# Kernel optimization log

Measured on AMD Instinct MI355X. Metric: run time of the kernel, lower is better.

The kernel has to match this reference:

```python
import jax, jax.numpy as jnp
import numpy as np

B, D, H, W = 32, 64, 32, 32   # batch, laten_dim, latent spatial dims
K = 2048                      # codebook_size


def setup_inputs() -> dict:
    key = jax.random.key(0)
    k1, k2 = jax.random.split(key)
    laten = jax.random.normal(k1, (B, D, H, W), dtype=jnp.float32)
    codebook = jax.random.normal(k2, (K, D), dtype=jnp.float32)
    return {"laten": laten, "codebook": codebook}


def reference(laten, codebook):
    # Faithful jax translation of VQVAE.quant_laten.
    b, c, h, w = laten.shape
    # (b, c, h, w) -> (b*h*w, c)
    x = jnp.transpose(laten, (0, 2, 3, 1)).reshape(-1, c)  # (N, D)
    # avoids materializing the (N, K, D) broadcast intermediate.
    x_sq = jnp.sum(x * x, axis=-1, keepdims=True)          # (N, 1)
    e_sq = jnp.sum(codebook * codebook, axis=-1)           # (K,)
    l2_distance = (x_sq - 2.0 * (x @ codebook.T) + e_sq) / c  # (N, K)
    closest_idx_2d = jnp.argmin(l2_distance, axis=-1).reshape(b, h, w)
    # gather + permute(0, 3, 1, 2)
    quant_laten = jnp.transpose(codebook[closest_idx_2d], (0, 3, 1, 2))
    return closest_idx_2d, quant_laten
```

## Files before the change

### kernel.cpp

```cpp
#include <hip/hip_runtime.h>

#define N_PIX 32768
#define DIM   64
#define KCODE 2048

typedef __attribute__((ext_vector_type(8))) short bf16x8;
typedef __attribute__((ext_vector_type(4))) float f32x4;

__device__ inline unsigned short f2bf(float v) {
    unsigned int u = __float_as_uint(v);
    return (unsigned short)((u + 0x7FFFu + ((u >> 16) & 1u)) >> 16);
}
__device__ inline float bf2f(unsigned short b) {
    return __uint_as_float(((unsigned int)b) << 16);
}

__global__ __launch_bounds__(256)
void convert_b_kernel(const float* __restrict__ cb, unsigned short* __restrict__ Bg,
                      float* __restrict__ esq) {
    const int t   = blockIdx.x * 256 + threadIdx.x;
    const int n   = t >> 4;
    const int sub = t & 15;
    const int ntile = n >> 4, ni = n & 15;

    const float4 v = *(const float4*)(cb + (size_t)n * DIM + sub * 4);

    unsigned int h01, h23, m01, m23, l01, l23;
    {
        unsigned short h, m, l;
        float r1;
        h = f2bf(v.x); r1 = v.x - bf2f(h); m = f2bf(r1); l = f2bf(r1 - bf2f(m));
        h01 = h;       m01 = m;       l01 = l;
        h = f2bf(v.y); r1 = v.y - bf2f(h); m = f2bf(r1); l = f2bf(r1 - bf2f(m));
        h01 |= (unsigned int)h << 16; m01 |= (unsigned int)m << 16; l01 |= (unsigned int)l << 16;
        h = f2bf(v.z); r1 = v.z - bf2f(h); m = f2bf(r1); l = f2bf(r1 - bf2f(m));
        h23 = h;       m23 = m;       l23 = l;
        h = f2bf(v.w); r1 = v.w - bf2f(h); m = f2bf(r1); l = f2bf(r1 - bf2f(m));
        h23 |= (unsigned int)h << 16; m23 |= (unsigned int)m << 16; l23 |= (unsigned int)l << 16;
    }

    float s = (v.x * v.x + v.y * v.y) + (v.z * v.z + v.w * v.w);
#pragma unroll
    for (int mk = 1; mk < 16; mk <<= 1) s += __shfl_xor(s, mk, 16);
    if (sub == 0) esq[n] = s;

    char* outb = (char*)Bg;
    const size_t u = ((((size_t)ntile) * 8 + (sub >> 1)) << 8) + ni * 16 + (sub & 1) * 8;
    uint2 hw2 = {h01, h23}, mw2 = {m01, m23}, lw2 = {l01, l23};
    *(uint2*)(outb + u)          = hw2;
    *(uint2*)(outb + 262144 + u) = mw2;
    *(uint2*)(outb + 524288 + u) = lw2;
}

#define DO_PASS(APL, BPL)                                                    \
    _Pragma("unroll") for (int ks = 0; ks < 2; ++ks)                         \
    _Pragma("unroll") for (int mt = 0; mt < 2; ++mt)                         \
        acc[mt] = __builtin_amdgcn_mfma_f32_16x16x32_bf16(                   \
            af[APL][mt][ks], bfr[BPL][ks], acc[mt], 0, 0, 0);

#define RELOAD(PL, JN)                                                       \
    if ((JN) < 32) {                                                         \
      const char* gb = bp0 + (size_t)(JN) * 2048 + (size_t)(PL) * 262144;    \
      bfr[PL][0] = *(const bf16x8*)(gb);                                     \
      bfr[PL][1] = *(const bf16x8*)(gb + 1024);                              \
    }

#define ITER(J)                                                              \
  {                                                                          \
    f32x4 acc[2];                                                            \
    acc[0] = f32x4{0.f, 0.f, 0.f, 0.f};                                      \
    acc[1] = f32x4{0.f, 0.f, 0.f, 0.f};                                      \
    __builtin_amdgcn_s_setprio(1);                                           \
    DO_PASS(0, 2)                                                            \
    RELOAD(2, (J) + 1)                                                       \
    DO_PASS(2, 0)                                                            \
    DO_PASS(1, 1)                                                            \
    DO_PASS(0, 1)                                                            \
    RELOAD(1, (J) + 1)                                                       \
    DO_PASS(1, 0)                                                            \
    DO_PASS(0, 0)                                                            \
    RELOAD(0, (J) + 1)                                                       \
    __builtin_amdgcn_s_setprio(0);                                           \
    const int n = wn * 512 + (J) * 16 + col;                                 \
    const float e = esqS[n];                                                 \
    _Pragma("unroll") for (int mt = 0; mt < 2; ++mt)                         \
    _Pragma("unroll") for (int r = 0; r < 4; ++r) {                          \
      float d = fmaf(-2.f, acc[mt][r], e);                                   \
      if (d < best[mt][r]) { best[mt][r] = d; bidx[mt][r] = n; }             \
    }                                                                        \
  }

__global__ __launch_bounds__(512, 4)
void dist_fused_kernel(const float* __restrict__ laten,
                       const unsigned short* __restrict__ Bg,
                       const float* __restrict__ esq,
                       const float* __restrict__ cb,
                       float* __restrict__ out0, float* __restrict__ out1) {
    __shared__ __align__(16) char ring[24576];
    __shared__ float esqS[2048];

    const int tid  = threadIdx.x;
    const int lane = tid & 63;
    const int wave = tid >> 6;
    const int wm   = wave & 1;
    const int wn   = wave >> 1;
    const int quad = lane >> 4, col = lane & 15;
    const int bx = blockIdx.x;
    const int bb = bx >> 4, hw0 = (bx & 15) * 64;

    const char* BgB = (const char*)Bg;
    const char* bp0 = BgB + (size_t)(wn * 32) * 2048 + lane * 16;

    {
        const int p = tid & 63, dg = tid >> 6;
        const float* srcA = laten + (size_t)bb * 65536 + (size_t)dg * 8192 + hw0 + p;
        const int mt = p >> 4, mi = p & 15;
        alignas(16) unsigned short hv[8], mv[8], lv[8];
#pragma unroll
        for (int j = 0; j < 8; ++j) {
            float v = srcA[(size_t)j << 10];
            unsigned short h = f2bf(v);
            float r1 = v - bf2f(h);
            unsigned short m = f2bf(r1);
            unsigned short l = f2bf(r1 - bf2f(m));
            hv[j] = h; mv[j] = m; lv[j] = l;
        }
        int u = ((mt * 8 + dg) << 8) + mi * 16;
        *(uint4*)(ring + u)         = *(uint4*)hv;
        *(uint4*)(ring + 8192 + u)  = *(uint4*)mv;
        *(uint4*)(ring + 16384 + u) = *(uint4*)lv;
    }
    *(float4*)(esqS + tid * 4) = *(const float4*)(esq + tid * 4);
    __syncthreads();

    bf16x8 af[3][2][2];
#pragma unroll
    for (int pl = 0; pl < 3; ++pl)
#pragma unroll
        for (int mt = 0; mt < 2; ++mt)
#pragma unroll
            for (int ks = 0; ks < 2; ++ks)
                af[pl][mt][ks] = *(const bf16x8*)(ring + pl * 8192
                    + (((wm * 2 + mt) * 8 + ks * 4 + quad) << 8) + col * 16);
    __syncthreads();

    bf16x8 bfr[3][2];
    RELOAD(2, 0)
    RELOAD(0, 0)
    RELOAD(1, 0)

    float best[2][4];
    int   bidx[2][4];
#pragma unroll
    for (int mt = 0; mt < 2; ++mt)
#pragma unroll
        for (int r = 0; r < 4; ++r) { best[mt][r] = 3.4e38f; bidx[mt][r] = 0; }

    for (int j = 0; j < 32; ++j) ITER(j)

    float* redD = (float*)ring;
    int*   redI = (int*)(ring + 1024);
    int*   idxF = (int*)(ring + 2048);
#pragma unroll
    for (int mt = 0; mt < 2; ++mt)
#pragma unroll
        for (int r = 0; r < 4; ++r) {
            float d = best[mt][r];
            int   i = bidx[mt][r];
#pragma unroll
            for (int m = 1; m < 16; m <<= 1) {
                float od = __shfl_xor(d, m, 16);
                int   oi = __shfl_xor(i, m, 16);
                if (od < d || (od == d && oi < i)) { d = od; i = oi; }
            }
            if (col == 0) {
                int row = wm * 32 + mt * 16 + quad * 4 + r;
                redD[row * 4 + wn] = d;
                redI[row * 4 + wn] = i;
            }
        }
    __syncthreads();

    if (tid < 64) {
        float bd = redD[tid * 4]; int bi = redI[tid * 4];
#pragma unroll
        for (int w = 1; w < 4; ++w) {
            float d = redD[tid * 4 + w]; int i = redI[tid * 4 + w];
            if (d < bd || (d == bd && i < bi)) { bd = d; bi = i; }
        }
        out0[bx * 64 + tid] = (float)bi;
        idxF[tid] = bi;
    }
    __syncthreads();

    const int p = tid & 63, dg = tid >> 6;
    const int idx = idxF[p];
    const float4* srcr = (const float4*)(cb + ((size_t)idx << 6) + dg * 8);
    float* o = out1 + (size_t)bb * 65536 + (size_t)dg * 8192 + hw0 + p;
    float4 v0 = srcr[0], v1 = srcr[1];
    o[(size_t)0 << 10] = v0.x; o[(size_t)1 << 10] = v0.y;
    o[(size_t)2 << 10] = v0.z; o[(size_t)3 << 10] = v0.w;
    o[(size_t)4 << 10] = v1.x; o[(size_t)5 << 10] = v1.y;
    o[(size_t)6 << 10] = v1.z; o[(size_t)7 << 10] = v1.w;
}

extern "C" void kernel_launch(void* const* d_in, const int* in_sizes, int n_in,
                              void* d_out, int out_size, void* d_ws, size_t ws_size,
                              hipStream_t stream) {
    const float* laten = (const float*)d_in[0];
    const float* cb    = (const float*)d_in[1];

    float* out0 = (float*)d_out;
    float* out1 = (float*)d_out + N_PIX;

    float* esq = (float*)d_ws;
    unsigned short* Bg = (unsigned short*)(esq + 2048);

    convert_b_kernel<<<128, 256, 0, stream>>>(cb, Bg, esq);

    dist_fused_kernel<<<512, 512, 0, stream>>>(laten, Bg, esq, cb, out0, out1);
}
```

Measured before the change: 104.6 us.

## Switch distance GEMM to 32x32x16 MFMA with direct register A-fragment loading

Replaces the 16x16x32 bf16 MFMA tiling with 32x32x16 MFMA, so each wave computes a 32x32 tile per iteration with two split accumulators that are summed before the argmin update. The A operand (split into three bf16 planes) is now built straight into registers from global memory, without staging through a shared-memory ring, which removes one shared-memory round trip and a barrier. Launch bounds occupancy is lowered from 4 to 2 to make room for the larger accumulators and fragments. The argmin reduction is reworked for the 32-lane layout. It trades occupancy and register pressure for fewer MFMA issues and more reuse per instruction.

```diff
diff --git a/kernel.cpp b/kernel.cpp
--- a/kernel.cpp
+++ b/kernel.cpp
@@ -4,8 +4,8 @@
 #define DIM   64
 #define KCODE 2048
 
-typedef __attribute__((ext_vector_type(8))) short bf16x8;
-typedef __attribute__((ext_vector_type(4))) float f32x4;
+typedef __attribute__((ext_vector_type(8)))  short bf16x8;
+typedef __attribute__((ext_vector_type(16))) float f32x16;
 
 __device__ inline unsigned short f2bf(float v) {
     unsigned int u = __float_as_uint(v);
@@ -53,23 +53,21 @@
 }
 
 #define DO_PASS(APL, BPL)                                                    \
-    _Pragma("unroll") for (int ks = 0; ks < 2; ++ks)                         \
-    _Pragma("unroll") for (int mt = 0; mt < 2; ++mt)                         \
-        acc[mt] = __builtin_amdgcn_mfma_f32_16x16x32_bf16(                   \
-            af[APL][mt][ks], bfr[BPL][ks], acc[mt], 0, 0, 0);
+    _Pragma("unroll") for (int ks = 0; ks < 4; ++ks)                         \
+        acc[ks & 1] = __builtin_amdgcn_mfma_f32_32x32x16_bf16(               \
+            af[APL][ks], bfr[BPL][ks], acc[ks & 1], 0, 0, 0);
 
 #define RELOAD(PL, JN)                                                       \
-    if ((JN) < 32) {                                                         \
-      const char* gb = bp0 + (size_t)(JN) * 2048 + (size_t)(PL) * 262144;    \
-      bfr[PL][0] = *(const bf16x8*)(gb);                                     \
-      bfr[PL][1] = *(const bf16x8*)(gb + 1024);                              \
+    if ((JN) < 16) {                                                         \
+      _Pragma("unroll") for (int ks = 0; ks < 4; ++ks)                       \
+        bfr[PL][ks] = *(const bf16x8*)(bp0 + (size_t)(JN) * 4096             \
+                                       + ks * 512 + (size_t)(PL) * 262144);  \
     }
 
 #define ITER(J)                                                              \
   {                                                                          \
-    f32x4 acc[2];                                                            \
-    acc[0] = f32x4{0.f, 0.f, 0.f, 0.f};                                      \
-    acc[1] = f32x4{0.f, 0.f, 0.f, 0.f};                                      \
+    f32x16 acc[2];                                                           \
+    _Pragma("unroll") for (int z = 0; z < 16; ++z) { acc[0][z] = 0.f; acc[1][z] = 0.f; } \
     __builtin_amdgcn_s_setprio(1);                                           \
     DO_PASS(0, 2)                                                            \
     RELOAD(2, (J) + 1)                                                       \
@@ -81,104 +79,94 @@
     DO_PASS(0, 0)                                                            \
     RELOAD(0, (J) + 1)                                                       \
     __builtin_amdgcn_s_setprio(0);                                           \
-    const int n = wn * 512 + (J) * 16 + col;                                 \
-    const float e = esqS[n];                                                 \
-    _Pragma("unroll") for (int mt = 0; mt < 2; ++mt)                         \
-    _Pragma("unroll") for (int r = 0; r < 4; ++r) {                          \
-      float d = fmaf(-2.f, acc[mt][r], e);                                   \
-      if (d < best[mt][r]) { best[mt][r] = d; bidx[mt][r] = n; }             \
+    const int n = wn * 512 + (J) * 32 + (lane & 31);                         \
+    const float e = esqF[n];                                                 \
+    _Pragma("unroll") for (int r = 0; r < 16; ++r) {                         \
+      float s2 = acc[0][r] + acc[1][r];                                      \
+      float d = fmaf(-2.f, s2, e);                                           \
+      if (d < best[r]) { best[r] = d; bidx[r] = n; }                         \
     }                                                                        \
   }
 
-__global__ __launch_bounds__(512, 4)
+__global__ __launch_bounds__(512, 2)
 void dist_fused_kernel(const float* __restrict__ laten,
                        const unsigned short* __restrict__ Bg,
                        const float* __restrict__ esq,
                        const float* __restrict__ cb,
                        float* __restrict__ out0, float* __restrict__ out1) {
-    __shared__ __align__(16) char ring[24576];
-    __shared__ float esqS[2048];
+    __shared__ float esqF[2048];
+    __shared__ float redD[256];
+    __shared__ int   redI[256];
+    __shared__ int   idxF[64];
 
     const int tid  = threadIdx.x;
     const int lane = tid & 63;
     const int wave = tid >> 6;
     const int wm   = wave & 1;
     const int wn   = wave >> 1;
-    const int quad = lane >> 4, col = lane & 15;
+    const int c31  = lane & 31;
+    const int hi   = lane >> 5;
     const int bx = blockIdx.x;
     const int bb = bx >> 4, hw0 = (bx & 15) * 64;
 
     const char* BgB = (const char*)Bg;
-    const char* bp0 = BgB + (size_t)(wn * 32) * 2048 + lane * 16;
-
+    const char* bp0 = BgB + (size_t)wn * 65536 + (size_t)(c31 >> 4) * 2048
+                    + (size_t)hi * 256 + (size_t)(c31 & 15) * 16;
+
+    bf16x8 af[3][4];
     {
-        const int p = tid & 63, dg = tid >> 6;
-        const float* srcA = laten + (size_t)bb * 65536 + (size_t)dg * 8192 + hw0 + p;
-        const int mt = p >> 4, mi = p & 15;
-        alignas(16) unsigned short hv[8], mv[8], lv[8];
-#pragma unroll
-        for (int j = 0; j < 8; ++j) {
-            float v = srcA[(size_t)j << 10];
-            unsigned short h = f2bf(v);
-            float r1 = v - bf2f(h);
-            unsigned short m = f2bf(r1);
-            unsigned short l = f2bf(r1 - bf2f(m));
-            hv[j] = h; mv[j] = m; lv[j] = l;
-        }
-        int u = ((mt * 8 + dg) << 8) + mi * 16;
-        *(uint4*)(ring + u)         = *(uint4*)hv;
-        *(uint4*)(ring + 8192 + u)  = *(uint4*)mv;
-        *(uint4*)(ring + 16384 + u) = *(uint4*)lv;
-    }
-    *(float4*)(esqS + tid * 4) = *(const float4*)(esq + tid * 4);
+        const int p = wm * 32 + c31;
+#pragma unroll
+        for (int ks = 0; ks < 4; ++ks) {
+            const float* srcA = laten + (size_t)bb * 65536
+                              + (size_t)(ks * 16 + hi * 8) * 1024 + hw0 + p;
+            bf16x8 hv, mv, lv;
+#pragma unroll
+            for (int j = 0; j < 8; ++j) {
+                float v = srcA[(size_t)j << 10];
+                unsigned short h = f2bf(v);
+                float r1 = v - bf2f(h);
+                unsigned short m = f2bf(r1);
+                unsigned short l = f2bf(r1 - bf2f(m));
+                hv[j] = (short)h; mv[j] = (short)m; lv[j] = (short)l;
+            }
+            af[0][ks] = hv;
+            af[1][ks] = mv;
+            af[2][ks] = lv;
+        }
+    }
+
+    *(float4*)(esqF + tid * 4) = *(const float4*)(esq + tid * 4);
     __syncthreads();
 
-    bf16x8 af[3][2][2];
-#pragma unroll
-    for (int pl = 0; pl < 3; ++pl)
-#pragma unroll
-        for (int mt = 0; mt < 2; ++mt)
-#pragma unroll
-            for (int ks = 0; ks < 2; ++ks)
-                af[pl][mt][ks] = *(const bf16x8*)(ring + pl * 8192
-                    + (((wm * 2 + mt) * 8 + ks * 4 + quad) << 8) + col * 16);
-    __syncthreads();
-
-    bf16x8 bfr[3][2];
+    bf16x8 bfr[3][4];
     RELOAD(2, 0)
     RELOAD(0, 0)
     RELOAD(1, 0)
 
-    float best[2][4];
-    int   bidx[2][4];
-#pragma unroll
-    for (int mt = 0; mt < 2; ++mt)
-#pragma unroll
-        for (int r = 0; r < 4; ++r) { best[mt][r] = 3.4e38f; bidx[mt][r] = 0; }
-
-    for (int j = 0; j < 32; ++j) ITER(j)
-
-    float* redD = (float*)ring;
-    int*   redI = (int*)(ring + 1024);
-    int*   idxF = (int*)(ring + 2048);
-#pragma unroll
-    for (int mt = 0; mt < 2; ++mt)
-#pragma unroll
-        for (int r = 0; r < 4; ++r) {
-            float d = best[mt][r];
-            int   i = bidx[mt][r];
-#pragma unroll
-            for (int m = 1; m < 16; m <<= 1) {
-                float od = __shfl_xor(d, m, 16);
-                int   oi = __shfl_xor(i, m, 16);
-                if (od < d || (od == d && oi < i)) { d = od; i = oi; }
-            }
-            if (col == 0) {
-                int row = wm * 32 + mt * 16 + quad * 4 + r;
-                redD[row * 4 + wn] = d;
-                redI[row * 4 + wn] = i;
-            }
-        }
+    float best[16];
+    int   bidx[16];
+#pragma unroll
+    for (int r = 0; r < 16; ++r) { best[r] = 3.4e38f; bidx[r] = 0; }
+
+    for (int j = 0; j < 16; ++j) ITER(j)
+
+#pragma unroll
+    for (int r = 0; r < 16; ++r) {
+        float d = best[r];
+        int   i = bidx[r];
+#pragma unroll
+        for (int m = 1; m < 32; m <<= 1) {
+            float od = __shfl_xor(d, m, 32);
+            int   oi = __shfl_xor(i, m, 32);
+            if (od < d || (od == d && oi < i)) { d = od; i = oi; }
+        }
+        if (c31 == 0) {
+            int p = wm * 32 + (r & 3) + 8 * (r >> 2) + 4 * hi;
+            redD[p * 4 + wn] = d;
+            redI[p * 4 + wn] = i;
+        }
+    }
     __syncthreads();
 
     if (tid < 64) {
```

Measured after the change: 123.0 us. +17.7%, slower.

## Load A fragments directly to registers, split accumulators, and stagger codebook walk per wave

Applied to the files above, without the earlier changes.

The A operand is now built straight into MFMA register fragments from global memory, which removes the LDS staging ring and one barrier. Each iteration keeps two independent accumulators, one per k-slice, to shorten MFMA dependency chains. Each wave group starts its codebook walk at a different tile offset to spread global and L2 access. The argmin gains an explicit lower-index tie-break so results stay deterministic under the rotated order. The direct loads are strided and uncoalesced, and the extra accumulators add register pressure.

```diff
diff --git a/kernel.cpp b/kernel.cpp
--- a/kernel.cpp
+++ b/kernel.cpp
@@ -55,38 +55,42 @@
 #define DO_PASS(APL, BPL)                                                    \
     _Pragma("unroll") for (int ks = 0; ks < 2; ++ks)                         \
     _Pragma("unroll") for (int mt = 0; mt < 2; ++mt)                         \
-        acc[mt] = __builtin_amdgcn_mfma_f32_16x16x32_bf16(                   \
-            af[APL][mt][ks], bfr[BPL][ks], acc[mt], 0, 0, 0);
+        acc[mt][ks] = __builtin_amdgcn_mfma_f32_16x16x32_bf16(               \
+            af[APL][mt][ks], bfr[BPL][ks], acc[mt][ks], 0, 0, 0);
 
 #define RELOAD(PL, JN)                                                       \
-    if ((JN) < 32) {                                                         \
+    {                                                                        \
       const char* gb = bp0 + (size_t)(JN) * 2048 + (size_t)(PL) * 262144;    \
       bfr[PL][0] = *(const bf16x8*)(gb);                                     \
       bfr[PL][1] = *(const bf16x8*)(gb + 1024);                              \
     }
 
-#define ITER(J)                                                              \
+#define ITER(J, JN, DOREL)                                                   \
   {                                                                          \
-    f32x4 acc[2];                                                            \
-    acc[0] = f32x4{0.f, 0.f, 0.f, 0.f};                                      \
-    acc[1] = f32x4{0.f, 0.f, 0.f, 0.f};                                      \
+    f32x4 acc[2][2];                                                         \
+    _Pragma("unroll") for (int mt = 0; mt < 2; ++mt)                         \
+    _Pragma("unroll") for (int ks = 0; ks < 2; ++ks)                         \
+        acc[mt][ks] = f32x4{0.f, 0.f, 0.f, 0.f};                             \
     __builtin_amdgcn_s_setprio(1);                                           \
     DO_PASS(0, 2)                                                            \
-    RELOAD(2, (J) + 1)                                                       \
+    if (DOREL) RELOAD(2, JN)                                                 \
     DO_PASS(2, 0)                                                            \
     DO_PASS(1, 1)                                                            \
     DO_PASS(0, 1)                                                            \
-    RELOAD(1, (J) + 1)                                                       \
+    if (DOREL) RELOAD(1, JN)                                                 \
     DO_PASS(1, 0)                                                            \
     DO_PASS(0, 0)                                                            \
-    RELOAD(0, (J) + 1)                                                       \
+    if (DOREL) RELOAD(0, JN)                                                 \
     __builtin_amdgcn_s_setprio(0);                                           \
     const int n = wn * 512 + (J) * 16 + col;                                 \
-    const float e = esqS[n];                                                 \
+    const float e = esqF[n];                                                 \
     _Pragma("unroll") for (int mt = 0; mt < 2; ++mt)                         \
     _Pragma("unroll") for (int r = 0; r < 4; ++r) {                          \
-      float d = fmaf(-2.f, acc[mt][r], e);                                   \
-      if (d < best[mt][r]) { best[mt][r] = d; bidx[mt][r] = n; }             \
+      float s2 = acc[mt][0][r] + acc[mt][1][r];                              \
+      float d = fmaf(-2.f, s2, e);                                           \
+      bool up = (d < best[mt][r]) ||                                         \
+                (d == best[mt][r] && n < bidx[mt][r]);                       \
+      if (up) { best[mt][r] = d; bidx[mt][r] = n; }                          \
     }                                                                        \
   }
 
@@ -96,8 +100,10 @@
                        const float* __restrict__ esq,
                        const float* __restrict__ cb,
                        float* __restrict__ out0, float* __restrict__ out1) {
-    __shared__ __align__(16) char ring[24576];
-    __shared__ float esqS[2048];
+    __shared__ float esqF[2048];
+    __shared__ float redD[256];
+    __shared__ int   redI[256];
+    __shared__ int   idxF[64];
 
     const int tid  = threadIdx.x;
     const int lane = tid & 63;
@@ -111,43 +117,37 @@
     const char* BgB = (const char*)Bg;
     const char* bp0 = BgB + (size_t)(wn * 32) * 2048 + lane * 16;
 
-    {
-        const int p = tid & 63, dg = tid >> 6;
-        const float* srcA = laten + (size_t)bb * 65536 + (size_t)dg * 8192 + hw0 + p;
-        const int mt = p >> 4, mi = p & 15;
-        alignas(16) unsigned short hv[8], mv[8], lv[8];
-#pragma unroll
-        for (int j = 0; j < 8; ++j) {
-            float v = srcA[(size_t)j << 10];
-            unsigned short h = f2bf(v);
-            float r1 = v - bf2f(h);
-            unsigned short m = f2bf(r1);
-            unsigned short l = f2bf(r1 - bf2f(m));
-            hv[j] = h; mv[j] = m; lv[j] = l;
+    bf16x8 af[3][2][2];
+#pragma unroll
+    for (int mt = 0; mt < 2; ++mt)
+#pragma unroll
+        for (int ks = 0; ks < 2; ++ks) {
+            const float* srcA = laten + (size_t)bb * 65536
+                              + (size_t)((ks * 4 + quad) * 8) * 1024
+                              + hw0 + wm * 32 + mt * 16 + col;
+            bf16x8 hv, mv, lv;
+#pragma unroll
+            for (int j = 0; j < 8; ++j) {
+                float v = srcA[(size_t)j << 10];
+                unsigned short h = f2bf(v);
+                float r1 = v - bf2f(h);
+                unsigned short m = f2bf(r1);
+                unsigned short l = f2bf(r1 - bf2f(m));
+                hv[j] = (short)h; mv[j] = (short)m; lv[j] = (short)l;
+            }
+            af[0][mt][ks] = hv;
+            af[1][mt][ks] = mv;
+            af[2][mt][ks] = lv;
         }
-        int u = ((mt * 8 + dg) << 8) + mi * 16;
-        *(uint4*)(ring + u)         = *(uint4*)hv;
-        *(uint4*)(ring + 8192 + u)  = *(uint4*)mv;
-        *(uint4*)(ring + 16384 + u) = *(uint4*)lv;
-    }
-    *(float4*)(esqS + tid * 4) = *(const float4*)(esq + tid * 4);
+
+    *(float4*)(esqF + tid * 4) = *(const float4*)(esq + tid * 4);
     __syncthreads();
 
-    bf16x8 af[3][2][2];
-#pragma unroll
-    for (int pl = 0; pl < 3; ++pl)
-#pragma unroll
-        for (int mt = 0; mt < 2; ++mt)
-#pragma unroll
-            for (int ks = 0; ks < 2; ++ks)
-                af[pl][mt][ks] = *(const bf16x8*)(ring + pl * 8192
-                    + (((wm * 2 + mt) * 8 + ks * 4 + quad) << 8) + col * 16);
-    __syncthreads();
-
+    const int j0 = wn * 8;
     bf16x8 bfr[3][2];
-    RELOAD(2, 0)
-    RELOAD(0, 0)
-    RELOAD(1, 0)
+    RELOAD(2, j0)
+    RELOAD(0, j0)
+    RELOAD(1, j0)
 
     float best[2][4];
     int   bidx[2][4];
@@ -156,11 +156,13 @@
 #pragma unroll
         for (int r = 0; r < 4; ++r) { best[mt][r] = 3.4e38f; bidx[mt][r] = 0; }
 
-    for (int j = 0; j < 32; ++j) ITER(j)
-
-    float* redD = (float*)ring;
-    int*   redI = (int*)(ring + 1024);
-    int*   idxF = (int*)(ring + 2048);
+#pragma unroll 4
+    for (int t = 0; t < 32; ++t) {
+        const int j  = (t + j0) & 31;
+        const int jn = (j + 1) & 31;
+        ITER(j, jn, t < 31)
+    }
+
 #pragma unroll
     for (int mt = 0; mt < 2; ++mt)
 #pragma unroll
```

New measurement: 184.3 us. 1.76x slower.
